# Performance work log

Hardware: AMD Instinct MI355X
Metric: run time of the kernel (lower is better)

Reference implementation:

```python
import jax, jax.numpy as jnp
import numpy as np

B, S, D, H = 4, 1024, 1024, 16
HD = D // H  # 64
NEG = -10000000.0


def setup_inputs() -> dict:
    key = jax.random.key(0)
    ks = jax.random.split(key, 8)
    x = jax.random.normal(ks[0], (B, S, D), dtype=jnp.float32)
    adj = jax.random.randint(ks[1], (B, S, S), 0, 2).astype(jnp.float32)
    scale = 1.0 / np.sqrt(D)
    Wq = jax.random.normal(ks[2], (D, D), dtype=jnp.float32) * scale
    bq = jnp.zeros((D,), dtype=jnp.float32)
    Wk = jax.random.normal(ks[3], (D, D), dtype=jnp.float32) * scale
    bk = jnp.zeros((D,), dtype=jnp.float32)
    Wv = jax.random.normal(ks[4], (D, D), dtype=jnp.float32) * scale
    bv = jnp.zeros((D,), dtype=jnp.float32)
    return {"x": x, "adj": adj, "Wq": Wq, "bq": bq, "Wk": Wk, "bk": bk, "Wv": Wv, "bv": bv}


def reference(x, adj, Wq, bq, Wk, bk, Wv, bv):
    # QKV projections, split into heads: [B,S,D] -> [B,H,S,HD]
    def heads(t):
        return t.reshape(B, S, H, HD).transpose(0, 2, 1, 3)

    q = heads(x @ Wq + bq)
    k = heads(x @ Wk + bk)
    v = heads(x @ Wv + bv)

    # scaled scores [B,H,S,S]
    scores = jnp.einsum('bhqd,bhkd->bhqk', q, k) / jnp.sqrt(jnp.asarray(HD, x.dtype))
    # adjacency mask: 0 where adj>=0.5 else -1e7, broadcast over heads
    mask_add = jnp.where(adj < 0.5, jnp.asarray(NEG, x.dtype), jnp.asarray(0.0, x.dtype))
    scores = scores + mask_add[:, None, :, :]

    probs = jax.nn.softmax(scores, axis=-1)
    ctx = jnp.einsum('bhqk,bhkd->bhqd', probs, v)  # [B,H,S,HD]
    ctx = ctx.transpose(0, 2, 1, 3).reshape(B, S, D)
    h = jax.nn.relu(ctx)
    return (h, adj)
```

## Files before the change

kernel.cpp:

```cpp
#include <hip/hip_runtime.h>

constexpr int Bn  = 4;
constexpr int Sn  = 1024;
constexpr int Dn  = 1024;
constexpr int Hn  = 16;
constexpr int HDn = 64;

using short8   = __attribute__((ext_vector_type(8))) short;
using float4v  = __attribute__((ext_vector_type(4))) float;
using float16v = __attribute__((ext_vector_type(16))) float;

__device__ __forceinline__ ushort f2bf(float f) {
    union { float f; unsigned u; } v; v.f = f;
    unsigned r = v.u + 0x7fff + ((v.u >> 16) & 1);
    return (ushort)(r >> 16);
}

__device__ __forceinline__ void gload16(const void* g, void* l) {
    __builtin_amdgcn_global_load_lds(
        (const __attribute__((address_space(1))) void*)g,
        (__attribute__((address_space(3))) void*)l, 16, 0, 0);
}

__global__ __launch_bounds__(256) void prep(
    const float* __restrict__ x,
    const float* __restrict__ Wq, const float* __restrict__ Wk,
    const float* __restrict__ Wv, const float* __restrict__ adj,
    ushort* __restrict__ xb, ushort* __restrict__ Wt, uint* __restrict__ Mb)
{
    const int bx  = blockIdx.x;
    const int tid = threadIdx.x;
    __shared__ __align__(16) ushort T[64 * 72];

    if (bx < 2048) {
        const size_t i = ((size_t)bx * 256 + tid) * 8;
        float4 a = *(const float4*)&x[i];
        float4 b = *(const float4*)&x[i + 4];
        ushort o[8] = {f2bf(a.x), f2bf(a.y), f2bf(a.z), f2bf(a.w),
                       f2bf(b.x), f2bf(b.y), f2bf(b.z), f2bf(b.w)};
        *(uint4*)&xb[i] = *(const uint4*)o;
    } else if (bx < 2816) {
        const int idx = bx - 2048;
        const int which = idx >> 8, rem = idx & 255;
        const float* __restrict__ W = (which == 0) ? Wq : (which == 1) ? Wk : Wv;
        ushort* __restrict__ O = Wt + (size_t)which * Dn * Dn;
        const int k0 = (rem & 15) * 64, n0 = (rem >> 4) * 64;

        const int kl = tid >> 4, nl = (tid & 15) * 4;
#pragma unroll
        for (int p = 0; p < 4; ++p) {
            float4 w4 = *(const float4*)&W[(size_t)(k0 + p * 16 + kl) * Dn + n0 + nl];
            T[(nl + 0) * 72 + p * 16 + kl] = f2bf(w4.x);
            T[(nl + 1) * 72 + p * 16 + kl] = f2bf(w4.y);
            T[(nl + 2) * 72 + p * 16 + kl] = f2bf(w4.z);
            T[(nl + 3) * 72 + p * 16 + kl] = f2bf(w4.w);
        }
        __syncthreads();
        const int nr = tid >> 2, kc = (tid & 3) * 16;
        uint4 u0 = *(const uint4*)&T[nr * 72 + kc];
        uint4 u1 = *(const uint4*)&T[nr * 72 + kc + 8];
        *(uint4*)&O[(size_t)(n0 + nr) * Dn + k0 + kc]     = u0;
        *(uint4*)&O[(size_t)(n0 + nr) * Dn + k0 + kc + 8] = u1;
    } else {
        const int rid  = (bx - 2816) * 256 + tid;
        const int lane = rid & 63;
        const int w    = (rid >> 6) & 3;
        const int kt   = (rid >> 8) & 15;
        const int qt   = (rid >> 12) & 7;
        const int b    = rid >> 15;
        const int col  = lane & 31, hi = lane >> 5;
        const int q    = qt * 128 + w * 32 + col;
        const float* arow = adj + ((size_t)b * Sn + q) * Sn + kt * 64;

        uint words[16];
#pragma unroll
        for (int mt = 0; mt < 2; ++mt)
#pragma unroll
            for (int pr = 0; pr < 8; ++pr) {
                const int r0 = 2 * pr;
                const int k0l = mt * 32 + (r0 & 3) + 8 * (r0 >> 2) + 4 * hi;
                float2 a = *(const float2*)&arow[k0l];
                words[mt * 8 + pr] = (a.x >= 0.5f ? 0x0000FFFFu : 0u) |
                                     (a.y >= 0.5f ? 0xFFFF0000u : 0u);
            }
        uint* dst = Mb + (size_t)rid * 16;
#pragma unroll
        for (int c = 0; c < 4; ++c)
            *(uint4*)&dst[c * 4] = make_uint4(words[c*4], words[c*4+1], words[c*4+2], words[c*4+3]);
    }
}

__global__ __launch_bounds__(256) void qkv_gemm(
    const ushort* __restrict__ xb, const ushort* __restrict__ Wt,
    const float* __restrict__ bq, const float* __restrict__ bk,
    const float* __restrict__ bv,
    ushort* __restrict__ Qb, ushort* __restrict__ Kb, ushort* __restrict__ Vb)
{
    const int which = blockIdx.z;
    const ushort* __restrict__ Bw   = Wt + (size_t)which * Dn * Dn;
    const float* __restrict__  bias = (which == 0) ? bq : (which == 1) ? bk : bv;
    ushort* __restrict__       Out  = (which == 0) ? Qb : (which == 1) ? Kb : Vb;
    const float scale = (which == 0) ? 0.18033688011112042f : 1.0f;

    const int n0   = blockIdx.x * 128;
    const int m0   = blockIdx.y * 128;
    const int tid  = threadIdx.x;
    const int wave = tid >> 6;
    const int lane = tid & 63;
    const int wm   = wave >> 1;
    const int wn   = wave & 1;

    __shared__ __align__(16) ushort As[128 * 32];
    __shared__ __align__(16) ushort Bs[128 * 32];

    const int L0 = wave * 64 + lane;
    const int r0s = L0 >> 2, c0s = (L0 & 3) * 8;
    const int L1 = L0 + 256;
    const int r1s = L1 >> 2, c1s = (L1 & 3) * 8;

    const ushort* pA0 = &xb[(size_t)(m0 + r0s) * Dn + c0s];
    const ushort* pA1 = &xb[(size_t)(m0 + r1s) * Dn + c1s];
    const ushort* pB0 = &Bw[(size_t)(n0 + r0s) * Dn + c0s];
    const ushort* pB1 = &Bw[(size_t)(n0 + r1s) * Dn + c1s];

    char* ldsA0 = (char*)As + wave * 1024;
    char* ldsA1 = (char*)As + wave * 1024 + 4096;
    char* ldsB0 = (char*)Bs + wave * 1024;
    char* ldsB1 = (char*)Bs + wave * 1024 + 4096;

    const int mlane = lane & 15;
    const int kg    = (lane >> 4) * 8;

    float4v acc[4][4];
    const float4v z4 = {0.f, 0.f, 0.f, 0.f};
#pragma unroll
    for (int i = 0; i < 4; ++i)
#pragma unroll
        for (int j = 0; j < 4; ++j) acc[i][j] = z4;

    for (int k0 = 0; k0 < Dn; k0 += 32) {
        __syncthreads();
        gload16(pA0, ldsA0);
        gload16(pA1, ldsA1);
        gload16(pB0, ldsB0);
        gload16(pB1, ldsB1);
        pA0 += 32; pA1 += 32; pB0 += 32; pB1 += 32;
        __syncthreads();

        short8 af[4], bf[4];
#pragma unroll
        for (int i = 0; i < 4; ++i)
            af[i] = *(const short8*)&As[(wm * 64 + i * 16 + mlane) * 32 + kg];
#pragma unroll
        for (int j = 0; j < 4; ++j)
            bf[j] = *(const short8*)&Bs[(wn * 64 + j * 16 + mlane) * 32 + kg];
#pragma unroll
        for (int i = 0; i < 4; ++i)
#pragma unroll
            for (int j = 0; j < 4; ++j)
                acc[i][j] = __builtin_amdgcn_mfma_f32_16x16x32_bf16(af[i], bf[j], acc[i][j], 0, 0, 0);
    }

    const int rb  = (lane >> 4) * 4;
    const int col = lane & 15;
#pragma unroll
    for (int j = 0; j < 4; ++j) {
        const int n  = n0 + wn * 64 + j * 16 + col;
        const float bias_n = bias[n];
        const int h  = n >> 6;
        const int hd = n & 63;
#pragma unroll
        for (int i = 0; i < 4; ++i) {
#pragma unroll
            for (int r = 0; r < 4; ++r) {
                const int m = m0 + wm * 64 + i * 16 + rb + r;
                const int b = m >> 10;
                const int s = m & 1023;
                size_t addr;
                if (which == 2)
                    addr = (((size_t)(b * Hn + h)) * HDn + hd) * Sn + s;
                else
                    addr = (((size_t)(b * Hn + h)) * Sn + s) * HDn + hd;
                Out[addr] = f2bf((acc[i][j][r] + bias_n) * scale);
            }
        }
    }
}

__global__ __launch_bounds__(256, 2) void attn_mfma(
    const ushort* __restrict__ Q, const ushort* __restrict__ K,
    const ushort* __restrict__ Vt, const uint* __restrict__ Mw,
    float* __restrict__ out)
{
    const int qt = blockIdx.x, h = blockIdx.y, b = blockIdx.z;
    const int tid  = threadIdx.x;
    const int w    = tid >> 6, lane = tid & 63;
    const int col  = lane & 31, hi = lane >> 5;

    const size_t hb = ((size_t)(b * Hn + h)) * Sn * HDn;
    const ushort* Kg = K + hb;
    const ushort* Vg = Vt + hb;

    __shared__ __align__(16) ushort Ks[2][64 * 72];
    __shared__ __align__(16) ushort Vs[2][64 * 72];

    short8 qf[4];
#pragma unroll
    for (int kp = 0; kp < 4; ++kp)
        qf[kp] = *(const short8*)&Q[hb +
            (size_t)(qt * 128 + w * 32 + col) * HDn + kp * 16 + hi * 8];

    float16v o_[2];
#pragma unroll
    for (int dt = 0; dt < 2; ++dt)
#pragma unroll
        for (int r = 0; r < 16; ++r) o_[dt][r] = 0.f;
    float ls = 0.f;

    const int c0 = tid, c1 = tid + 256;
    const int la0 = (c0 >> 3) * 72 + (c0 & 7) * 8;
    const int la1 = (c1 >> 3) * 72 + (c1 & 7) * 8;

    uint4 k0 = *(const uint4*)&Kg[(size_t)(c0 >> 3) * HDn + (c0 & 7) * 8];
    uint4 k1 = *(const uint4*)&Kg[(size_t)(c1 >> 3) * HDn + (c1 & 7) * 8];
    uint4 v0 = *(const uint4*)&Vg[(size_t)(c0 >> 3) * Sn + (c0 & 7) * 8];
    uint4 v1 = *(const uint4*)&Vg[(size_t)(c1 >> 3) * Sn + (c1 & 7) * 8];
    *(uint4*)&Ks[0][la0] = k0;  *(uint4*)&Ks[0][la1] = k1;
    *(uint4*)&Vs[0][la0] = v0;  *(uint4*)&Vs[0][la1] = v1;
    __syncthreads();

    const uint* mbase = Mw + ((size_t)((b * 8 + qt) * 16) * 4 + w) * 1024 + lane * 16;

    for (int kt = 0; kt < 16; ++kt) {
        const int cur = kt & 1;
        if (kt < 15) {
            k0 = *(const uint4*)&Kg[(size_t)((kt + 1) * 64 + (c0 >> 3)) * HDn + (c0 & 7) * 8];
            k1 = *(const uint4*)&Kg[(size_t)((kt + 1) * 64 + (c1 >> 3)) * HDn + (c1 & 7) * 8];
            v0 = *(const uint4*)&Vg[(size_t)(c0 >> 3) * Sn + (kt + 1) * 64 + (c0 & 7) * 8];
            v1 = *(const uint4*)&Vg[(size_t)(c1 >> 3) * Sn + (kt + 1) * 64 + (c1 & 7) * 8];
        }
        const uint* mp = mbase + (size_t)kt * 4096;
        uint4 mk4[4];
        mk4[0] = *(const uint4*)(mp);
        mk4[1] = *(const uint4*)(mp + 4);
        mk4[2] = *(const uint4*)(mp + 8);
        mk4[3] = *(const uint4*)(mp + 12);
        const uint* mka = (const uint*)mk4;

#pragma unroll
        for (int mt = 0; mt < 2; ++mt) {
            float16v s_;
#pragma unroll
            for (int r = 0; r < 16; ++r) s_[r] = 0.f;
#pragma unroll
            for (int kp = 0; kp < 4; ++kp) {
                short8 ak = *(const short8*)&Ks[cur][(mt * 32 + col) * 72 + kp * 16 + hi * 8];
                s_ = __builtin_amdgcn_mfma_f32_32x32x16_bf16(ak, qf[kp], s_, 0, 0, 0);
            }

            unsigned up[8];
#pragma unroll
            for (int pr = 0; pr < 8; ++pr) {
                const unsigned e0 = __float_as_uint(exp2f(s_[2 * pr]))     + 0x8000u;
                const unsigned e1 = __float_as_uint(exp2f(s_[2 * pr + 1])) + 0x8000u;
                const unsigned u  = __builtin_amdgcn_perm(e1, e0, 0x07060302u) & mka[mt * 8 + pr];
                up[pr] = u;
                ls += __uint_as_float(u << 16) + __uint_as_float(u & 0xffff0000u);
            }

#pragma unroll
            for (int kh = 0; kh < 2; ++kh) {
                const unsigned a0 = up[kh * 4 + 0], a1 = up[kh * 4 + 1];
                const unsigned a2 = up[kh * 4 + 2], a3 = up[kh * 4 + 3];
                const unsigned t0 = (unsigned)__shfl_xor((int)(hi ? a0 : a2), 32, 64);
                const unsigned t1 = (unsigned)__shfl_xor((int)(hi ? a1 : a3), 32, 64);
                union { short8 s; unsigned u[4]; } f;
                f.u[0] = hi ? t0 : a0;
                f.u[1] = hi ? t1 : a1;
                f.u[2] = hi ? a2 : t0;
                f.u[3] = hi ? a3 : t1;
                const int kp = mt * 2 + kh;
#pragma unroll
                for (int dt = 0; dt < 2; ++dt) {
                    short8 av = *(const short8*)&Vs[cur][(dt * 32 + col) * 72 + kp * 16 + hi * 8];
                    o_[dt] = __builtin_amdgcn_mfma_f32_32x32x16_bf16(av, f.s, o_[dt], 0, 0, 0);
                }
            }
        }

        if (kt < 15) {
            const int nxt = cur ^ 1;
            *(uint4*)&Ks[nxt][la0] = k0;  *(uint4*)&Ks[nxt][la1] = k1;
            *(uint4*)&Vs[nxt][la0] = v0;  *(uint4*)&Vs[nxt][la1] = v1;
        }
        __syncthreads();
    }

    float l = ls + (float)__shfl_xor((float)ls, 32, 64);
    const float inv = 1.0f / l;
    const int q = qt * 128 + w * 32 + col;
    float* op = &out[((size_t)b * Sn + q) * Dn + h * 64];
#pragma unroll
    for (int dt = 0; dt < 2; ++dt)
#pragma unroll
        for (int rg = 0; rg < 4; ++rg) {
            const int d = dt * 32 + rg * 8 + hi * 4;
            float4 o4;
            o4.x = fmaxf(o_[dt][rg * 4 + 0] * inv, 0.0f);
            o4.y = fmaxf(o_[dt][rg * 4 + 1] * inv, 0.0f);
            o4.z = fmaxf(o_[dt][rg * 4 + 2] * inv, 0.0f);
            o4.w = fmaxf(o_[dt][rg * 4 + 3] * inv, 0.0f);
            *(float4*)&op[d] = o4;
        }
}

extern "C" void kernel_launch(void* const* d_in, const int* in_sizes, int n_in,
                              void* d_out, int out_size, void* d_ws, size_t ws_size,
                              hipStream_t stream)
{
    const float* x   = (const float*)d_in[0];
    const float* adj = (const float*)d_in[1];
    const float* Wq  = (const float*)d_in[2];
    const float* bq  = (const float*)d_in[3];
    const float* Wk  = (const float*)d_in[4];
    const float* bk  = (const float*)d_in[5];
    const float* Wv  = (const float*)d_in[6];
    const float* bv  = (const float*)d_in[7];
    float* out = (float*)d_out;

    ushort* xb = (ushort*)d_ws;
    ushort* Wt = xb + (size_t)Bn * Sn * Dn;
    ushort* Qb = Wt + (size_t)3 * Dn * Dn;
    ushort* Kb = Qb + (size_t)Bn * Hn * Sn * HDn;
    ushort* Vb = Kb + (size_t)Bn * Hn * Sn * HDn;
    uint*   Mb = (uint*)(Vb + (size_t)Bn * Hn * Sn * HDn);

    prep<<<dim3(3328), 256, 0, stream>>>(x, Wq, Wk, Wv, adj, xb, Wt, Mb);

    qkv_gemm<<<dim3(Dn / 128, (Bn * Sn) / 128, 3), 256, 0, stream>>>(
        xb, Wt, bq, bk, bv, Qb, Kb, Vb);

    attn_mfma<<<dim3(8, Hn, Bn), 256, 0, stream>>>(Qb, Kb, Vb, Mb, out);

    hipMemcpyAsync(out + (size_t)Bn * Sn * Dn, adj,
                   (size_t)Bn * Sn * Sn * sizeof(float),
                   hipMemcpyDeviceToDevice, stream);
}
```

Measured before the change: 191.0 us.

## Fuse adj copy into mask prep, transpose V via LDS, split-K attention waves

The separate adj memcpy is folded into the prep kernel, so adj is read once to build the mask bitwords and to write the passthrough output. The mask build now stages through shared memory, which allows coalesced loads. The V projection epilogue transposes through LDS so global stores are vectorized rather than scattered 2-byte writes. Attention now uses twice as many blocks: pairs of waves split the key range and their partial outputs and row sums are combined through shared memory. This raises occupancy (launch bounds 4) at the cost of an extra reduction and idle waves at each kt step.

```diff
diff --git a/kernel.cpp b/kernel.cpp
--- a/kernel.cpp
+++ b/kernel.cpp
@@ -26,11 +26,13 @@
     const float* __restrict__ x,
     const float* __restrict__ Wq, const float* __restrict__ Wk,
     const float* __restrict__ Wv, const float* __restrict__ adj,
-    ushort* __restrict__ xb, ushort* __restrict__ Wt, uint* __restrict__ Mb)
+    ushort* __restrict__ xb, ushort* __restrict__ Wt, uint* __restrict__ Mb,
+    float* __restrict__ out)
 {
     const int bx  = blockIdx.x;
     const int tid = threadIdx.x;
     __shared__ __align__(16) ushort T[64 * 72];
+    __shared__ char msk[32][64];
 
     if (bx < 2048) {
         const size_t i = ((size_t)bx * 256 + tid) * 8;
@@ -62,31 +64,42 @@
         *(uint4*)&O[(size_t)(n0 + nr) * Dn + k0 + kc]     = u0;
         *(uint4*)&O[(size_t)(n0 + nr) * Dn + k0 + kc + 8] = u1;
     } else {
-        const int rid  = (bx - 2816) * 256 + tid;
-        const int lane = rid & 63;
-        const int w    = (rid >> 6) & 3;
-        const int kt   = (rid >> 8) & 15;
-        const int qt   = (rid >> 12) & 7;
-        const int b    = rid >> 15;
-        const int col  = lane & 31, hi = lane >> 5;
-        const int q    = qt * 128 + w * 32 + col;
-        const float* arow = adj + ((size_t)b * Sn + q) * Sn + kt * 64;
-
-        uint words[16];
-#pragma unroll
-        for (int mt = 0; mt < 2; ++mt)
-#pragma unroll
-            for (int pr = 0; pr < 8; ++pr) {
+        const int idx = bx - 2816;
+        const int b = idx >> 5, qsub = idx & 31;
+        const float* abase = adj + ((size_t)b * Sn + qsub * 32) * Sn;
+        float* ocopy = out + (size_t)Bn * Sn * Dn + ((size_t)b * Sn + qsub * 32) * Sn;
+
+        const int row = tid >> 3, cc = (tid & 7) * 8;
+        const int lane = tid & 63, part = tid >> 6;
+        const int col = lane & 31, hi = lane >> 5;
+
+        for (int kt = 0; kt < 16; ++kt) {
+            const size_t off = (size_t)row * Sn + kt * 64 + cc;
+            float4 a0 = *(const float4*)&abase[off];
+            float4 a1 = *(const float4*)&abase[off + 4];
+            *(float4*)&ocopy[off]     = a0;
+            *(float4*)&ocopy[off + 4] = a1;
+            char* mrow = &msk[row][cc];
+            mrow[0] = a0.x >= 0.5f; mrow[1] = a0.y >= 0.5f;
+            mrow[2] = a0.z >= 0.5f; mrow[3] = a0.w >= 0.5f;
+            mrow[4] = a1.x >= 0.5f; mrow[5] = a1.y >= 0.5f;
+            mrow[6] = a1.z >= 0.5f; mrow[7] = a1.w >= 0.5f;
+            __syncthreads();
+
+            uint w4[4];
+#pragma unroll
+            for (int i = 0; i < 4; ++i) {
+                const int prg = part * 4 + i;
+                const int mt = prg >> 3, pr = prg & 7;
                 const int r0 = 2 * pr;
-                const int k0l = mt * 32 + (r0 & 3) + 8 * (r0 >> 2) + 4 * hi;
-                float2 a = *(const float2*)&arow[k0l];
-                words[mt * 8 + pr] = (a.x >= 0.5f ? 0x0000FFFFu : 0u) |
-                                     (a.y >= 0.5f ? 0xFFFF0000u : 0u);
+                const int kl = mt * 32 + (r0 & 3) + 8 * (r0 >> 2) + 4 * hi;
+                w4[i] = (msk[col][kl]     ? 0x0000FFFFu : 0u) |
+                        (msk[col][kl + 1] ? 0xFFFF0000u : 0u);
             }
-        uint* dst = Mb + (size_t)rid * 16;
-#pragma unroll
-        for (int c = 0; c < 4; ++c)
-            *(uint4*)&dst[c * 4] = make_uint4(words[c*4], words[c*4+1], words[c*4+2], words[c*4+3]);
+            const size_t rid = ((size_t)(b * 32 + qsub) * 16 + kt) * 64 + lane;
+            *(uint4*)&Mb[rid * 16 + part * 4] = make_uint4(w4[0], w4[1], w4[2], w4[3]);
+            __syncthreads();
+        }
     }
 }
 
@@ -110,8 +123,9 @@
     const int wm   = wave >> 1;
     const int wn   = wave & 1;
 
-    __shared__ __align__(16) ushort As[128 * 32];
-    __shared__ __align__(16) ushort Bs[128 * 32];
+    __shared__ __align__(16) ushort pool[128 * 136];
+    ushort* As = pool;
+    ushort* Bs = pool + 128 * 32;
 
     const int L0 = wave * 64 + lane;
     const int r0s = L0 >> 2, c0s = (L0 & 3) * 8;
@@ -163,31 +177,53 @@
 
     const int rb  = (lane >> 4) * 4;
     const int col = lane & 15;
-#pragma unroll
-    for (int j = 0; j < 4; ++j) {
-        const int n  = n0 + wn * 64 + j * 16 + col;
-        const float bias_n = bias[n];
-        const int h  = n >> 6;
-        const int hd = n & 63;
-#pragma unroll
-        for (int i = 0; i < 4; ++i) {
-#pragma unroll
-            for (int r = 0; r < 4; ++r) {
-                const int m = m0 + wm * 64 + i * 16 + rb + r;
-                const int b = m >> 10;
-                const int s = m & 1023;
-                size_t addr;
-                if (which == 2)
-                    addr = (((size_t)(b * Hn + h)) * HDn + hd) * Sn + s;
-                else
-                    addr = (((size_t)(b * Hn + h)) * Sn + s) * HDn + hd;
-                Out[addr] = f2bf((acc[i][j][r] + bias_n) * scale);
+
+    if (which == 2) {
+        __syncthreads();
+        ushort* C2 = pool;
+#pragma unroll
+        for (int j = 0; j < 4; ++j) {
+            const int n = wn * 64 + j * 16 + col;
+            const float bias_n = bias[n0 + n];
+#pragma unroll
+            for (int i = 0; i < 4; ++i) {
+                ushort h4[4];
+#pragma unroll
+                for (int r = 0; r < 4; ++r) h4[r] = f2bf(acc[i][j][r] + bias_n);
+                *(uint2*)&C2[n * 136 + wm * 64 + i * 16 + rb] = *(const uint2*)h4;
             }
         }
-    }
-}
-
-__global__ __launch_bounds__(256, 2) void attn_mfma(
+        __syncthreads();
+        const int n  = tid >> 1, mh = (tid & 1) * 64;
+        const int gn = n0 + n, hh = gn >> 6, hd = gn & 63;
+        const int bb = m0 >> 10, s0 = (m0 & 1023) + mh;
+        ushort* dst = &Out[(((size_t)(bb * Hn + hh)) * HDn + hd) * Sn + s0];
+#pragma unroll
+        for (int c = 0; c < 8; ++c)
+            *(uint4*)&dst[c * 8] = *(const uint4*)&C2[n * 136 + mh + c * 8];
+    } else {
+#pragma unroll
+        for (int j = 0; j < 4; ++j) {
+            const int n  = n0 + wn * 64 + j * 16 + col;
+            const float bias_n = bias[n];
+            const int h  = n >> 6;
+            const int hd = n & 63;
+#pragma unroll
+            for (int i = 0; i < 4; ++i) {
+#pragma unroll
+                for (int r = 0; r < 4; ++r) {
+                    const int m = m0 + wm * 64 + i * 16 + rb + r;
+                    const int b = m >> 10;
+                    const int s = m & 1023;
+                    Out[(((size_t)(b * Hn + h)) * Sn + s) * HDn + hd] =
+                        f2bf((acc[i][j][r] + bias_n) * scale);
+                }
+            }
+        }
+    }
+}
+
+__global__ __launch_bounds__(256, 4) void attn_mfma(
     const ushort* __restrict__ Q, const ushort* __restrict__ K,
     const ushort* __restrict__ Vt, const uint* __restrict__ Mw,
     float* __restrict__ out)
@@ -196,6 +232,8 @@
     const int tid  = threadIdx.x;
     const int w    = tid >> 6, lane = tid & 63;
     const int col  = lane & 31, hi = lane >> 5;
+    const int jt   = w & 1, kh = w >> 1;
+    const int qsub = qt * 2 + jt;
 
     const size_t hb = ((size_t)(b * Hn + h)) * Sn * HDn;
     const ushort* Kg = K + hb;
@@ -208,7 +246,7 @@
 #pragma unroll
     for (int kp = 0; kp < 4; ++kp)
         qf[kp] = *(const short8*)&Q[hb +
-            (size_t)(qt * 128 + w * 32 + col) * HDn + kp * 16 + hi * 8];
+            (size_t)(qsub * 32 + col) * HDn + kp * 16 + hi * 8];
 
     float16v o_[2];
 #pragma unroll
@@ -229,7 +267,7 @@
     *(uint4*)&Vs[0][la0] = v0;  *(uint4*)&Vs[0][la1] = v1;
     __syncthreads();
 
-    const uint* mbase = Mw + ((size_t)((b * 8 + qt) * 16) * 4 + w) * 1024 + lane * 16;
+    const uint* mb0 = Mw + (((size_t)(b * 32 + qsub) * 16) * 64 + lane) * 16;
 
     for (int kt = 0; kt < 16; ++kt) {
         const int cur = kt & 1;
@@ -239,51 +277,54 @@
             v0 = *(const uint4*)&Vg[(size_t)(c0 >> 3) * Sn + (kt + 1) * 64 + (c0 & 7) * 8];
             v1 = *(const uint4*)&Vg[(size_t)(c1 >> 3) * Sn + (kt + 1) * 64 + (c1 & 7) * 8];
         }
-        const uint* mp = mbase + (size_t)kt * 4096;
-        uint4 mk4[4];
-        mk4[0] = *(const uint4*)(mp);
-        mk4[1] = *(const uint4*)(mp + 4);
-        mk4[2] = *(const uint4*)(mp + 8);
-        mk4[3] = *(const uint4*)(mp + 12);
-        const uint* mka = (const uint*)mk4;
-
-#pragma unroll
-        for (int mt = 0; mt < 2; ++mt) {
-            float16v s_;
-#pragma unroll
-            for (int r = 0; r < 16; ++r) s_[r] = 0.f;
-#pragma unroll
-            for (int kp = 0; kp < 4; ++kp) {
-                short8 ak = *(const short8*)&Ks[cur][(mt * 32 + col) * 72 + kp * 16 + hi * 8];
-                s_ = __builtin_amdgcn_mfma_f32_32x32x16_bf16(ak, qf[kp], s_, 0, 0, 0);
-            }
-
-            unsigned up[8];
-#pragma unroll
-            for (int pr = 0; pr < 8; ++pr) {
-                const unsigned e0 = __float_as_uint(exp2f(s_[2 * pr]))     + 0x8000u;
-                const unsigned e1 = __float_as_uint(exp2f(s_[2 * pr + 1])) + 0x8000u;
-                const unsigned u  = __builtin_amdgcn_perm(e1, e0, 0x07060302u) & mka[mt * 8 + pr];
-                up[pr] = u;
-                ls += __uint_as_float(u << 16) + __uint_as_float(u & 0xffff0000u);
-            }
-
-#pragma unroll
-            for (int kh = 0; kh < 2; ++kh) {
-                const unsigned a0 = up[kh * 4 + 0], a1 = up[kh * 4 + 1];
-                const unsigned a2 = up[kh * 4 + 2], a3 = up[kh * 4 + 3];
-                const unsigned t0 = (unsigned)__shfl_xor((int)(hi ? a0 : a2), 32, 64);
-                const unsigned t1 = (unsigned)__shfl_xor((int)(hi ? a1 : a3), 32, 64);
-                union { short8 s; unsigned u[4]; } f;
-                f.u[0] = hi ? t0 : a0;
-                f.u[1] = hi ? t1 : a1;
-                f.u[2] = hi ? a2 : t0;
-                f.u[3] = hi ? a3 : t1;
-                const int kp = mt * 2 + kh;
-#pragma unroll
-                for (int dt = 0; dt < 2; ++dt) {
-                    short8 av = *(const short8*)&Vs[cur][(dt * 32 + col) * 72 + kp * 16 + hi * 8];
-                    o_[dt] = __builtin_amdgcn_mfma_f32_32x32x16_bf16(av, f.s, o_[dt], 0, 0, 0);
+
+        if ((kt >> 3) == kh) {
+            const uint* mp = mb0 + (size_t)kt * 1024;
+            uint4 mk4[4];
+            mk4[0] = *(const uint4*)(mp);
+            mk4[1] = *(const uint4*)(mp + 4);
+            mk4[2] = *(const uint4*)(mp + 8);
+            mk4[3] = *(const uint4*)(mp + 12);
+            const uint* mka = (const uint*)mk4;
+
+#pragma unroll
+            for (int mt = 0; mt < 2; ++mt) {
+                float16v s_;
+#pragma unroll
+                for (int r = 0; r < 16; ++r) s_[r] = 0.f;
+#pragma unroll
+                for (int kp = 0; kp < 4; ++kp) {
+                    short8 ak = *(const short8*)&Ks[cur][(mt * 32 + col) * 72 + kp * 16 + hi * 8];
+                    s_ = __builtin_amdgcn_mfma_f32_32x32x16_bf16(ak, qf[kp], s_, 0, 0, 0);
+                }
+
+                unsigned up[8];
+#pragma unroll
+                for (int pr = 0; pr < 8; ++pr) {
+                    const unsigned e0 = __float_as_uint(exp2f(s_[2 * pr]))     + 0x8000u;
+                    const unsigned e1 = __float_as_uint(exp2f(s_[2 * pr + 1])) + 0x8000u;
+                    const unsigned u  = __builtin_amdgcn_perm(e1, e0, 0x07060302u) & mka[mt * 8 + pr];
+                    up[pr] = u;
+                    ls += __uint_as_float(u << 16) + __uint_as_float(u & 0xffff0000u);
+                }
+
+#pragma unroll
+                for (int kkh = 0; kkh < 2; ++kkh) {
+                    const unsigned a0 = up[kkh * 4 + 0], a1 = up[kkh * 4 + 1];
+                    const unsigned a2 = up[kkh * 4 + 2], a3 = up[kkh * 4 + 3];
+                    const unsigned t0 = (unsigned)__shfl_xor((int)(hi ? a0 : a2), 32, 64);
+                    const unsigned t1 = (unsigned)__shfl_xor((int)(hi ? a1 : a3), 32, 64);
+                    union { short8 s; unsigned u[4]; } f;
+                    f.u[0] = hi ? t0 : a0;
+                    f.u[1] = hi ? t1 : a1;
+                    f.u[2] = hi ? a2 : t0;
+                    f.u[3] = hi ? a3 : t1;
+                    const int kp = mt * 2 + kkh;
+#pragma unroll
+                    for (int dt = 0; dt < 2; ++dt) {
+                        short8 av = *(const short8*)&Vs[cur][(dt * 32 + col) * 72 + kp * 16 + hi * 8];
+                        o_[dt] = __builtin_amdgcn_mfma_f32_32x32x16_bf16(av, f.s, o_[dt], 0, 0, 0);
+                    }
                 }
             }
         }
@@ -296,22 +337,44 @@
         __syncthreads();
     }
 
-    float l = ls + (float)__shfl_xor((float)ls, 32, 64);
-    const float inv = 1.0f / l;
-    const int q = qt * 128 + w * 32 + col;
-    float* op = &out[((size_t)b * Sn + q) * Dn + h * 64];
-#pragma unroll
-    for (int dt = 0; dt < 2; ++dt)
-#pragma unroll
-        for (int rg = 0; rg < 4; ++rg) {
-            const int d = dt * 32 + rg * 8 + hi * 4;
-            float4 o4;
-            o4.x = fmaxf(o_[dt][rg * 4 + 0] * inv, 0.0f);
-            o4.y = fmaxf(o_[dt][rg * 4 + 1] * inv, 0.0f);
-            o4.z = fmaxf(o_[dt][rg * 4 + 2] * inv, 0.0f);
-            o4.w = fmaxf(o_[dt][rg * 4 + 3] * inv, 0.0f);
-            *(float4*)&op[d] = o4;
-        }
+    float* red = (float*)Ks;
+    if (kh == 1) {
+        float* p = red + (size_t)(jt * 64 + lane) * 36;
+#pragma unroll
+        for (int dt = 0; dt < 2; ++dt)
+#pragma unroll
+            for (int c = 0; c < 4; ++c)
+                *(float4*)&p[dt * 16 + c * 4] = make_float4(
+                    o_[dt][c * 4 + 0], o_[dt][c * 4 + 1],
+                    o_[dt][c * 4 + 2], o_[dt][c * 4 + 3]);
+        p[32] = ls;
+    }
+    __syncthreads();
+    if (kh == 0) {
+        const float* p = red + (size_t)(jt * 64 + lane) * 36;
+#pragma unroll
+        for (int dt = 0; dt < 2; ++dt)
+#pragma unroll
+            for (int r = 0; r < 16; ++r) o_[dt][r] += p[dt * 16 + r];
+        ls += p[32];
+
+        float l = ls + (float)__shfl_xor((float)ls, 32, 64);
+        const float inv = 1.0f / l;
+        const int q = qsub * 32 + col;
+        float* op = &out[((size_t)b * Sn + q) * Dn + h * 64];
+#pragma unroll
+        for (int dt = 0; dt < 2; ++dt)
+#pragma unroll
+            for (int rg = 0; rg < 4; ++rg) {
+                const int d = dt * 32 + rg * 8 + hi * 4;
+                float4 o4;
+                o4.x = fmaxf(o_[dt][rg * 4 + 0] * inv, 0.0f);
+                o4.y = fmaxf(o_[dt][rg * 4 + 1] * inv, 0.0f);
+                o4.z = fmaxf(o_[dt][rg * 4 + 2] * inv, 0.0f);
+                o4.w = fmaxf(o_[dt][rg * 4 + 3] * inv, 0.0f);
+                *(float4*)&op[d] = o4;
+            }
+    }
 }
 
 extern "C" void kernel_launch(void* const* d_in, const int* in_sizes, int n_in,
@@ -335,14 +398,10 @@
     ushort* Vb = Kb + (size_t)Bn * Hn * Sn * HDn;
     uint*   Mb = (uint*)(Vb + (size_t)Bn * Hn * Sn * HDn);
 
-    prep<<<dim3(3328), 256, 0, stream>>>(x, Wq, Wk, Wv, adj, xb, Wt, Mb);
+    prep<<<dim3(2944), 256, 0, stream>>>(x, Wq, Wk, Wv, adj, xb, Wt, Mb, out);
 
     qkv_gemm<<<dim3(Dn / 128, (Bn * Sn) / 128, 3), 256, 0, stream>>>(
         xb, Wt, bq, bk, bv, Qb, Kb, Vb);
 
-    attn_mfma<<<dim3(8, Hn, Bn), 256, 0, stream>>>(Qb, Kb, Vb, Mb, out);
-
-    hipMemcpyAsync(out + (size_t)Bn * Sn * Dn, adj,
-                   (size_t)Bn * Sn * Sn * sizeof(float),
-                   hipMemcpyDeviceToDevice, stream);
-}
+    attn_mfma<<<dim3(16, Hn, Bn), 256, 0, stream>>>(Qb, Kb, Vb, Mb, out);
+}
```

After: 222.7 us. +16.6%, slower.
